# Performance work log

Measured on AMD Instinct MI355X. Metric: run time of the kernel, lower is better.

## Reference

```python
import jax, jax.numpy as jnp
import numpy as np

B, N, DH, DX, DQ, DE = 8, 256, 32, 3, 1, 8
H1, H2 = 32, 32
DIN = 2 * (DX + DH + DQ) + DE  # 80
TOL = 1e-5


def setup_inputs() -> dict:
    key = jax.random.key(0)
    ks = jax.random.split(key, 11)
    s1 = 1.0 / np.sqrt(DIN)
    s2 = 1.0 / np.sqrt(H1)
    s3 = 1.0 / np.sqrt(H2)
    return {
        "h": jax.random.normal(ks[0], (B, N, DH), jnp.float32),
        "e": jax.random.uniform(ks[1], (B, N, N, DE), jnp.float32),
        "x": jax.random.normal(ks[2], (B, N, DX), jnp.float32),
        "q": jax.random.normal(ks[3], (B, N, DQ), jnp.float32),
        "mask": jax.random.uniform(ks[4], (B, N, N, 1), jnp.float32),
        "W1": jax.random.normal(ks[5], (DIN, H1), jnp.float32) * s1,
        "b1": jnp.zeros((H1,), jnp.float32),
        "W2": jax.random.normal(ks[6], (H1, H2), jnp.float32) * s2,
        "b2": jnp.zeros((H2,), jnp.float32),
        "W3": jax.random.normal(ks[7], (H2, 1), jnp.float32) * s3,
        "b3": jnp.zeros((1,), jnp.float32),
    }


def reference(h, e, x, q, mask, W1, b1, W2, b2, W3, b3):
    natom = e.shape[1]
    # is_near: any edge feature above tolerance for pair (i,j)
    clip = jnp.clip(e, TOL, 1e5)
    is_near = (jnp.max(clip, axis=-1) != TOL).astype(jnp.float32)  # [B,N,N]
    m = jnp.max(mask, axis=-1)  # [B,N,N]

    def mlp(z):  # [..., DIN] -> [...]
        z = jax.nn.relu(z @ W1 + b1)
        z = jax.nn.relu(z @ W2 + b2)
        return (z @ W3 + b3)[..., 0]

    inp_atom = jnp.concatenate([x, h, q], axis=-1)  # [B,N,F]
    F = inp_atom.shape[-1]
    inp_i = jnp.broadcast_to(inp_atom[:, :, None, :], (inp_atom.shape[0], natom, natom, F))
    inp_j = jnp.transpose(inp_i, (0, 2, 1, 3))

    elec_ij = mlp(jnp.concatenate([inp_i, inp_j, e], axis=-1))  # [B,N,N]
    elec_ji = mlp(jnp.concatenate([inp_j, inp_i, e], axis=-1))  # [B,N,N]

    antisym = 0.5 * (elec_ij - elec_ji) * m * is_near
    q = q + jnp.sum(antisym, axis=2)[..., None]  # [B,N,1]
    return q
```

## Files before the change

kernel.cpp:

```cpp
#include <hip/hip_runtime.h>


#define NATOM 256
#define TOT_ATOMS 2048
#define ZS 40

typedef __bf16 bf16x8 __attribute__((ext_vector_type(8)));
typedef float  f32x16 __attribute__((ext_vector_type(16)));

__device__ __forceinline__ unsigned int pk2(float a, float b) {
    unsigned short lo = __builtin_bit_cast(unsigned short, (__bf16)a);
    unsigned short hi = __builtin_bit_cast(unsigned short, (__bf16)b);
    return (unsigned int)lo | ((unsigned int)hi << 16);
}

__global__ __launch_bounds__(256) void atom_proj_kernel(
    const float* __restrict__ x, const float* __restrict__ h,
    const float* __restrict__ q, const float* __restrict__ W1,
    const float* __restrict__ b1, float* __restrict__ P)
{
    const int a  = threadIdx.x >> 5;
    const int u  = threadIdx.x & 31;
    const int n0 = blockIdx.x * 8;

    __shared__ float sd[8][37];
    for (int idx = threadIdx.x; idx < 8 * 36; idx += 256) {
        const int aa = idx / 36, r = idx - aa * 36;
        const int n = n0 + aa;
        float v;
        if (r < 3)       v = x[n * 3 + r];
        else if (r < 35) v = h[n * 32 + (r - 3)];
        else             v = q[n];
        sd[aa][r] = v;
    }
    __syncthreads();

    float pa = 0.f, pb = b1[u];
#pragma unroll
    for (int r = 0; r < 36; ++r) {
        const float d = sd[a][r];
        pa += d * W1[r * 32 + u];
        pb += d * W1[(36 + r) * 32 + u];
    }
    const int n = n0 + a;
    P[(size_t)n * 64 + u]      = pa;
    P[(size_t)n * 64 + 32 + u] = pb;
}

__global__ __launch_bounds__(256, 3) void pair_kernel(
    const float* __restrict__ e, const float* __restrict__ mask,
    const float* __restrict__ q, const float* __restrict__ P,
    const float* __restrict__ W1, const float* __restrict__ W2,
    const float* __restrict__ b2, const float* __restrict__ W3,
    float* __restrict__ out)
{
    const int row = blockIdx.x;
    const int b   = row >> 8;
    const int j   = threadIdx.x;
    const int col = (b << 8) + j;

    __shared__ unsigned short Zij[256 * ZS];
    __shared__ unsigned short Zji[256 * ZS];
    __shared__ unsigned short W2t[32 * ZS];
    __shared__ float g_lds[256];
    __shared__ float red[4];

    const float* ep = e + (size_t)(row * NATOM + j) * 8;
    const float4 ev0 = ((const float4*)ep)[0];
    const float4 ev1 = ((const float4*)ep)[1];
    float e8[8] = {ev0.x, ev0.y, ev0.z, ev0.w, ev1.x, ev1.y, ev1.z, ev1.w};
    const float m = mask[row * NATOM + j];
    float mx = e8[0];
#pragma unroll
    for (int k = 1; k < 8; ++k) mx = fmaxf(mx, e8[k]);
    const float near = (mx > 1e-5f) ? 1.0f : 0.0f;
    g_lds[j] = 0.5f * m * near;

    {
        const int u  = threadIdx.x >> 3;
        const int k0 = (threadIdx.x & 7) * 4;
        const unsigned int p0 = pk2(W2[(k0 + 0) * 32 + u], W2[(k0 + 1) * 32 + u]);
        const unsigned int p1 = pk2(W2[(k0 + 2) * 32 + u], W2[(k0 + 3) * 32 + u]);
        *(unsigned int*)&W2t[u * ZS + k0]     = p0;
        *(unsigned int*)&W2t[u * ZS + k0 + 2] = p1;
    }

    const float* Pi = P + (size_t)row * 64;
    const float* Pj = P + (size_t)col * 64;
#pragma unroll
    for (int kq = 0; kq < 8; ++kq) {
        const float4 paj4 = ((const float4*)Pj)[kq];
        const float4 pbj4 = ((const float4*)Pj)[8 + kq];
        const float* paj = (const float*)&paj4;
        const float* pbj = (const float*)&pbj4;
        float zij[4], zji[4];
#pragma unroll
        for (int kk = 0; kk < 4; ++kk) {
            const int k = kq * 4 + kk;
            float ez = 0.f;
#pragma unroll
            for (int de = 0; de < 8; ++de)
                ez += e8[de] * W1[(72 + de) * 32 + k];
            const float pai = Pi[k];
            const float pbi = Pi[32 + k];
            zij[kk] = fmaxf(pai + pbj[kk] + ez, 0.f);
            zji[kk] = fmaxf(paj[kk] + pbi + ez, 0.f);
        }
        const unsigned int i0 = pk2(zij[0], zij[1]), i1 = pk2(zij[2], zij[3]);
        const unsigned int j0 = pk2(zji[0], zji[1]), j1 = pk2(zji[2], zji[3]);
        *(uint2*)&Zij[j * ZS + kq * 4] = make_uint2(i0, i1);
        *(uint2*)&Zji[j * ZS + kq * 4] = make_uint2(j0, j1);
    }
    __syncthreads();

    const int wave = threadIdx.x >> 6;
    const int lane = threadIdx.x & 63;
    const int lo = lane & 31;
    const int h  = lane >> 5;

    const bf16x8 a0 = *(const bf16x8*)&W2t[lo * ZS + h * 8];
    const bf16x8 a1 = *(const bf16x8*)&W2t[lo * ZS + 16 + h * 8];

    float vacc = 0.f;
#pragma unroll
    for (int nt = 0; nt < 2; ++nt) {
        const int jt = (wave + nt * 4) * 32;
        const int zo = (jt + lo) * ZS + h * 8;
        f32x16 cij = {0.f}, cji = {0.f};
        {
            const bf16x8 bz0 = *(const bf16x8*)&Zij[zo];
            const bf16x8 bz1 = *(const bf16x8*)&Zij[zo + 16];
            cij = __builtin_amdgcn_mfma_f32_32x32x16_bf16(a0, bz0, cij, 0, 0, 0);
            cij = __builtin_amdgcn_mfma_f32_32x32x16_bf16(a1, bz1, cij, 0, 0, 0);
        }
        {
            const bf16x8 bz0 = *(const bf16x8*)&Zji[zo];
            const bf16x8 bz1 = *(const bf16x8*)&Zji[zo + 16];
            cji = __builtin_amdgcn_mfma_f32_32x32x16_bf16(a0, bz0, cji, 0, 0, 0);
            cji = __builtin_amdgcn_mfma_f32_32x32x16_bf16(a1, bz1, cji, 0, 0, 0);
        }
        float d = 0.f;
#pragma unroll
        for (int reg = 0; reg < 16; ++reg) {
            const int u0 = (reg & 3) + 8 * (reg >> 2);
            const float b2v = h ? b2[u0 + 4] : b2[u0];
            const float w3v = h ? W3[u0 + 4] : W3[u0];
            const float rij = fmaxf(cij[reg] + b2v, 0.f);
            const float rji = fmaxf(cji[reg] + b2v, 0.f);
            d += (rij - rji) * w3v;
        }
        d += __shfl_xor(d, 32, 64);
        vacc += d * g_lds[jt + lo];
    }

#pragma unroll
    for (int off = 1; off < 64; off <<= 1)
        vacc += __shfl_xor(vacc, off, 64);
    if (lane == 0) red[wave] = vacc;
    __syncthreads();
    if (threadIdx.x == 0)
        out[row] = q[row] + 0.5f * (red[0] + red[1] + red[2] + red[3]);
}

extern "C" void kernel_launch(void* const* d_in, const int* in_sizes, int n_in,
                              void* d_out, int out_size, void* d_ws, size_t ws_size,
                              hipStream_t stream)
{
    const float* h    = (const float*)d_in[0];
    const float* e    = (const float*)d_in[1];
    const float* x    = (const float*)d_in[2];
    const float* q    = (const float*)d_in[3];
    const float* mask = (const float*)d_in[4];
    const float* W1   = (const float*)d_in[5];
    const float* b1   = (const float*)d_in[6];
    const float* W2   = (const float*)d_in[7];
    const float* b2   = (const float*)d_in[8];
    const float* W3   = (const float*)d_in[9];

    float* P = (float*)d_ws;

    atom_proj_kernel<<<256, 256, 0, stream>>>(x, h, q, W1, b1, P);
    pair_kernel<<<TOT_ATOMS, 256, 0, stream>>>(e, mask, q, P, W1, W2, b2, W3,
                                               (float*)d_out);
}
```

Measured before the change: 107.2 us.

## Build MFMA B-operands directly in registers, removing LDS staging of hidden activations

The first-layer activations are now computed directly in the lane layout that the 32x32x16 bf16 MFMA expects, so they feed the matrix op from registers instead of going through LDS with a block barrier. W2 fragments are loaded straight from global memory per lane. The launch-bounds occupancy hint rises from 3 to 4 blocks. The cost is duplicated e/mask loads and P loads across lane halves, plus higher register pressure.

```diff
diff --git a/kernel.cpp b/kernel.cpp
--- a/kernel.cpp
+++ b/kernel.cpp
@@ -3,16 +3,9 @@
 
 #define NATOM 256
 #define TOT_ATOMS 2048
-#define ZS 40
 
 typedef __bf16 bf16x8 __attribute__((ext_vector_type(8)));
 typedef float  f32x16 __attribute__((ext_vector_type(16)));
-
-__device__ __forceinline__ unsigned int pk2(float a, float b) {
-    unsigned short lo = __builtin_bit_cast(unsigned short, (__bf16)a);
-    unsigned short hi = __builtin_bit_cast(unsigned short, (__bf16)b);
-    return (unsigned int)lo | ((unsigned int)hi << 16);
-}
 
 __global__ __launch_bounds__(256) void atom_proj_kernel(
     const float* __restrict__ x, const float* __restrict__ h,
@@ -47,98 +40,94 @@
     P[(size_t)n * 64 + 32 + u] = pb;
 }
 
-__global__ __launch_bounds__(256, 3) void pair_kernel(
+__global__ __launch_bounds__(256, 4) void pair_kernel(
     const float* __restrict__ e, const float* __restrict__ mask,
     const float* __restrict__ q, const float* __restrict__ P,
     const float* __restrict__ W1, const float* __restrict__ W2,
     const float* __restrict__ b2, const float* __restrict__ W3,
     float* __restrict__ out)
 {
-    const int row = blockIdx.x;
-    const int b   = row >> 8;
-    const int j   = threadIdx.x;
-    const int col = (b << 8) + j;
+    const int row  = blockIdx.x;
+    const int b    = row >> 8;
+    const int tid  = threadIdx.x;
+    const int wave = tid >> 6;
+    const int lane = tid & 63;
+    const int lo   = lane & 31;
+    const int h    = lane >> 5;
 
-    __shared__ unsigned short Zij[256 * ZS];
-    __shared__ unsigned short Zji[256 * ZS];
-    __shared__ unsigned short W2t[32 * ZS];
-    __shared__ float g_lds[256];
-    __shared__ float red[4];
-
-    const float* ep = e + (size_t)(row * NATOM + j) * 8;
-    const float4 ev0 = ((const float4*)ep)[0];
-    const float4 ev1 = ((const float4*)ep)[1];
-    float e8[8] = {ev0.x, ev0.y, ev0.z, ev0.w, ev1.x, ev1.y, ev1.z, ev1.w};
-    const float m = mask[row * NATOM + j];
-    float mx = e8[0];
+    bf16x8 A0, A1;
 #pragma unroll
-    for (int k = 1; k < 8; ++k) mx = fmaxf(mx, e8[k]);
-    const float near = (mx > 1e-5f) ? 1.0f : 0.0f;
-    g_lds[j] = 0.5f * m * near;
-
-    {
-        const int u  = threadIdx.x >> 3;
-        const int k0 = (threadIdx.x & 7) * 4;
-        const unsigned int p0 = pk2(W2[(k0 + 0) * 32 + u], W2[(k0 + 1) * 32 + u]);
-        const unsigned int p1 = pk2(W2[(k0 + 2) * 32 + u], W2[(k0 + 3) * 32 + u]);
-        *(unsigned int*)&W2t[u * ZS + k0]     = p0;
-        *(unsigned int*)&W2t[u * ZS + k0 + 2] = p1;
+    for (int t = 0; t < 8; ++t) {
+        A0[t] = (__bf16)W2[(h * 8 + t) * 32 + lo];
+        A1[t] = (__bf16)W2[(16 + h * 8 + t) * 32 + lo];
     }
 
     const float* Pi = P + (size_t)row * 64;
-    const float* Pj = P + (size_t)col * 64;
+    __shared__ float red[4];
+    float vacc = 0.f;
+
 #pragma unroll
-    for (int kq = 0; kq < 8; ++kq) {
-        const float4 paj4 = ((const float4*)Pj)[kq];
-        const float4 pbj4 = ((const float4*)Pj)[8 + kq];
-        const float* paj = (const float*)&paj4;
-        const float* pbj = (const float*)&pbj4;
-        float zij[4], zji[4];
+    for (int st = 0; st < 2; ++st) {
+        const int j    = (wave << 6) + (st << 5) + lo;
+        const int colj = (b << 8) + j;
+        const float* Pj = P + (size_t)colj * 64;
+
+        const float* ep = e + ((size_t)row * NATOM + j) * 8;
+        float e8[8];
+        *(float4*)&e8[0] = ((const float4*)ep)[0];
+        *(float4*)&e8[4] = ((const float4*)ep)[1];
+        const float m = mask[row * NATOM + j];
+        float mx = e8[0];
 #pragma unroll
-        for (int kk = 0; kk < 4; ++kk) {
-            const int k = kq * 4 + kk;
-            float ez = 0.f;
+        for (int k = 1; k < 8; ++k) mx = fmaxf(mx, e8[k]);
+        const float g = (mx > 1e-5f) ? 0.5f * m : 0.f;
+
+        f32x16 cij = {0.f}, cji = {0.f};
 #pragma unroll
-            for (int de = 0; de < 8; ++de)
-                ez += e8[de] * W1[(72 + de) * 32 + k];
-            const float pai = Pi[k];
-            const float pbi = Pi[32 + k];
-            zij[kk] = fmaxf(pai + pbj[kk] + ez, 0.f);
-            zji[kk] = fmaxf(paj[kk] + pbi + ez, 0.f);
+        for (int kb = 0; kb < 2; ++kb) {
+            const int k0 = kb * 16 + h * 8;
+            const float4 pai0 = *(const float4*)(Pi + k0);
+            const float4 pai1 = *(const float4*)(Pi + k0 + 4);
+            const float4 pbi0 = *(const float4*)(Pi + 32 + k0);
+            const float4 pbi1 = *(const float4*)(Pi + 32 + k0 + 4);
+            const float4 paj0 = *(const float4*)(Pj + k0);
+            const float4 paj1 = *(const float4*)(Pj + k0 + 4);
+            const float4 pbj0 = *(const float4*)(Pj + 32 + k0);
+            const float4 pbj1 = *(const float4*)(Pj + 32 + k0 + 4);
+
+            float ez[8] = {0.f, 0.f, 0.f, 0.f, 0.f, 0.f, 0.f, 0.f};
+#pragma unroll
+            for (int de = 0; de < 8; ++de) {
+                const float ev = e8[de];
+                const float4 wa = *(const float4*)(W1 + (72 + de) * 32 + k0);
+                const float4 wb = *(const float4*)(W1 + (72 + de) * 32 + k0 + 4);
+                ez[0] += ev * wa.x; ez[1] += ev * wa.y;
+                ez[2] += ev * wa.z; ez[3] += ev * wa.w;
+                ez[4] += ev * wb.x; ez[5] += ev * wb.y;
+                ez[6] += ev * wb.z; ez[7] += ev * wb.w;
+            }
+
+            bf16x8 Bij, Bji;
+#pragma unroll
+            for (int t = 0; t < 8; ++t) {
+                const float pai = (t < 4) ? ((const float*)&pai0)[t] : ((const float*)&pai1)[t - 4];
+                const float pbi = (t < 4) ? ((const float*)&pbi0)[t] : ((const float*)&pbi1)[t - 4];
+                const float paj = (t < 4) ? ((const float*)&paj0)[t] : ((const float*)&paj1)[t - 4];
+                const float pbj = (t < 4) ? ((const float*)&pbj0)[t] : ((const float*)&pbj1)[t - 4];
+                const float zij = fmaxf(pai + pbj + ez[t], 0.f);
+                const float zji = fmaxf(paj + pbi + ez[t], 0.f);
+                Bij[t] = (__bf16)zij;
+                Bji[t] = (__bf16)zji;
+            }
+            if (kb == 0) {
+                cij = __builtin_amdgcn_mfma_f32_32x32x16_bf16(A0, Bij, cij, 0, 0, 0);
+                cji = __builtin_amdgcn_mfma_f32_32x32x16_bf16(A0, Bji, cji, 0, 0, 0);
+            } else {
+                cij = __builtin_amdgcn_mfma_f32_32x32x16_bf16(A1, Bij, cij, 0, 0, 0);
+                cji = __builtin_amdgcn_mfma_f32_32x32x16_bf16(A1, Bji, cji, 0, 0, 0);
+            }
         }
-        const unsigned int i0 = pk2(zij[0], zij[1]), i1 = pk2(zij[2], zij[3]);
-        const unsigned int j0 = pk2(zji[0], zji[1]), j1 = pk2(zji[2], zji[3]);
-        *(uint2*)&Zij[j * ZS + kq * 4] = make_uint2(i0, i1);
-        *(uint2*)&Zji[j * ZS + kq * 4] = make_uint2(j0, j1);
-    }
-    __syncthreads();
 
-    const int wave = threadIdx.x >> 6;
-    const int lane = threadIdx.x & 63;
-    const int lo = lane & 31;
-    const int h  = lane >> 5;
-
-    const bf16x8 a0 = *(const bf16x8*)&W2t[lo * ZS + h * 8];
-    const bf16x8 a1 = *(const bf16x8*)&W2t[lo * ZS + 16 + h * 8];
-
-    float vacc = 0.f;
-#pragma unroll
-    for (int nt = 0; nt < 2; ++nt) {
-        const int jt = (wave + nt * 4) * 32;
-        const int zo = (jt + lo) * ZS + h * 8;
-        f32x16 cij = {0.f}, cji = {0.f};
-        {
-            const bf16x8 bz0 = *(const bf16x8*)&Zij[zo];
-            const bf16x8 bz1 = *(const bf16x8*)&Zij[zo + 16];
-            cij = __builtin_amdgcn_mfma_f32_32x32x16_bf16(a0, bz0, cij, 0, 0, 0);
-            cij = __builtin_amdgcn_mfma_f32_32x32x16_bf16(a1, bz1, cij, 0, 0, 0);
-        }
-        {
-            const bf16x8 bz0 = *(const bf16x8*)&Zji[zo];
-            const bf16x8 bz1 = *(const bf16x8*)&Zji[zo + 16];
-            cji = __builtin_amdgcn_mfma_f32_32x32x16_bf16(a0, bz0, cji, 0, 0, 0);
-            cji = __builtin_amdgcn_mfma_f32_32x32x16_bf16(a1, bz1, cji, 0, 0, 0);
-        }
         float d = 0.f;
 #pragma unroll
         for (int reg = 0; reg < 16; ++reg) {
@@ -150,7 +139,7 @@
             d += (rij - rji) * w3v;
         }
         d += __shfl_xor(d, 32, 64);
-        vacc += d * g_lds[jt + lo];
+        vacc += d * g;
     }
 
 #pragma unroll
@@ -158,7 +147,7 @@
         vacc += __shfl_xor(vacc, off, 64);
     if (lane == 0) red[wave] = vacc;
     __syncthreads();
-    if (threadIdx.x == 0)
+    if (tid == 0)
         out[row] = q[row] + 0.5f * (red[0] + red[1] + red[2] + red[3]);
 }
 
```

After: 315.4 us. +194.2%, slower.

## Swizzle unpadded Z tiles in LDS and load W2 fragments directly to registers

Applied to the files above, without the earlier changes.

Removes the padding from the Z row stride and applies an XOR swizzle to the 8-element chunks so the bf16x8 reads avoid LDS bank conflicts while using less shared memory. The transposed W2 staging in LDS is dropped. Each lane now builds its MFMA A operand straight from global W2 into registers. Occupancy is raised to 4 blocks per SIMD in launch bounds, which adds register pressure.

```diff
diff --git a/kernel.cpp b/kernel.cpp
--- a/kernel.cpp
+++ b/kernel.cpp
@@ -3,10 +3,13 @@
 
 #define NATOM 256
 #define TOT_ATOMS 2048
-#define ZS 40
+#define ZS 32
 
 typedef __bf16 bf16x8 __attribute__((ext_vector_type(8)));
 typedef float  f32x16 __attribute__((ext_vector_type(16)));
+typedef float  f32x4  __attribute__((ext_vector_type(4)));
+typedef unsigned int u32x2 __attribute__((ext_vector_type(2)));
+typedef unsigned int u32x4 __attribute__((ext_vector_type(4)));
 
 __device__ __forceinline__ unsigned int pk2(float a, float b) {
     unsigned short lo = __builtin_bit_cast(unsigned short, (__bf16)a);
@@ -47,7 +50,7 @@
     P[(size_t)n * 64 + 32 + u] = pb;
 }
 
-__global__ __launch_bounds__(256, 3) void pair_kernel(
+__global__ __launch_bounds__(256, 4) void pair_kernel(
     const float* __restrict__ e, const float* __restrict__ mask,
     const float* __restrict__ q, const float* __restrict__ P,
     const float* __restrict__ W1, const float* __restrict__ W2,
@@ -61,83 +64,82 @@
 
     __shared__ unsigned short Zij[256 * ZS];
     __shared__ unsigned short Zji[256 * ZS];
-    __shared__ unsigned short W2t[32 * ZS];
     __shared__ float g_lds[256];
     __shared__ float red[4];
 
-    const float* ep = e + (size_t)(row * NATOM + j) * 8;
-    const float4 ev0 = ((const float4*)ep)[0];
-    const float4 ev1 = ((const float4*)ep)[1];
-    float e8[8] = {ev0.x, ev0.y, ev0.z, ev0.w, ev1.x, ev1.y, ev1.z, ev1.w};
+    const float* ep = e + ((size_t)row * NATOM + j) * 8;
+    const f32x4 ea = *(const f32x4*)(ep);
+    const f32x4 eb = *(const f32x4*)(ep + 4);
     const float m = mask[row * NATOM + j];
-    float mx = e8[0];
-#pragma unroll
-    for (int k = 1; k < 8; ++k) mx = fmaxf(mx, e8[k]);
-    const float near = (mx > 1e-5f) ? 1.0f : 0.0f;
-    g_lds[j] = 0.5f * m * near;
-
-    {
-        const int u  = threadIdx.x >> 3;
-        const int k0 = (threadIdx.x & 7) * 4;
-        const unsigned int p0 = pk2(W2[(k0 + 0) * 32 + u], W2[(k0 + 1) * 32 + u]);
-        const unsigned int p1 = pk2(W2[(k0 + 2) * 32 + u], W2[(k0 + 3) * 32 + u]);
-        *(unsigned int*)&W2t[u * ZS + k0]     = p0;
-        *(unsigned int*)&W2t[u * ZS + k0 + 2] = p1;
-    }
+    const float mx = fmaxf(fmaxf(fmaxf(ea[0], ea[1]), fmaxf(ea[2], ea[3])),
+                           fmaxf(fmaxf(eb[0], eb[1]), fmaxf(eb[2], eb[3])));
+    g_lds[j] = (mx > 1e-5f) ? 0.5f * m : 0.f;
 
     const float* Pi = P + (size_t)row * 64;
     const float* Pj = P + (size_t)col * 64;
+    const int sw = (j >> 1) & 3;
 #pragma unroll
     for (int kq = 0; kq < 8; ++kq) {
-        const float4 paj4 = ((const float4*)Pj)[kq];
-        const float4 pbj4 = ((const float4*)Pj)[8 + kq];
-        const float* paj = (const float*)&paj4;
-        const float* pbj = (const float*)&pbj4;
+        const f32x4 paj = *(const f32x4*)(Pj + kq * 4);
+        const f32x4 pbj = *(const f32x4*)(Pj + 32 + kq * 4);
         float zij[4], zji[4];
 #pragma unroll
         for (int kk = 0; kk < 4; ++kk) {
             const int k = kq * 4 + kk;
             float ez = 0.f;
 #pragma unroll
-            for (int de = 0; de < 8; ++de)
-                ez += e8[de] * W1[(72 + de) * 32 + k];
+            for (int de = 0; de < 8; ++de) {
+                const float ev = (de < 4) ? ea[de] : eb[de - 4];
+                ez += ev * W1[(72 + de) * 32 + k];
+            }
             const float pai = Pi[k];
             const float pbi = Pi[32 + k];
             zij[kk] = fmaxf(pai + pbj[kk] + ez, 0.f);
             zji[kk] = fmaxf(paj[kk] + pbi + ez, 0.f);
         }
-        const unsigned int i0 = pk2(zij[0], zij[1]), i1 = pk2(zij[2], zij[3]);
-        const unsigned int j0 = pk2(zji[0], zji[1]), j1 = pk2(zji[2], zji[3]);
-        *(uint2*)&Zij[j * ZS + kq * 4] = make_uint2(i0, i1);
-        *(uint2*)&Zji[j * ZS + kq * 4] = make_uint2(j0, j1);
+        const int off = j * ZS + (((kq >> 1) ^ sw) << 3) + ((kq & 1) << 2);
+        *(u32x2*)&Zij[off] = (u32x2){ pk2(zij[0], zij[1]), pk2(zij[2], zij[3]) };
+        *(u32x2*)&Zji[off] = (u32x2){ pk2(zji[0], zji[1]), pk2(zji[2], zji[3]) };
     }
-    __syncthreads();
 
     const int wave = threadIdx.x >> 6;
     const int lane = threadIdx.x & 63;
-    const int lo = lane & 31;
-    const int h  = lane >> 5;
+    const int lo   = lane & 31;
+    const int h    = lane >> 5;
+    const int kA   = h * 8;
+    const u32x4 a0w = { pk2(W2[(kA + 0) * 32 + lo], W2[(kA + 1) * 32 + lo]),
+                        pk2(W2[(kA + 2) * 32 + lo], W2[(kA + 3) * 32 + lo]),
+                        pk2(W2[(kA + 4) * 32 + lo], W2[(kA + 5) * 32 + lo]),
+                        pk2(W2[(kA + 6) * 32 + lo], W2[(kA + 7) * 32 + lo]) };
+    const u32x4 a1w = { pk2(W2[(16 + kA + 0) * 32 + lo], W2[(16 + kA + 1) * 32 + lo]),
+                        pk2(W2[(16 + kA + 2) * 32 + lo], W2[(16 + kA + 3) * 32 + lo]),
+                        pk2(W2[(16 + kA + 4) * 32 + lo], W2[(16 + kA + 5) * 32 + lo]),
+                        pk2(W2[(16 + kA + 6) * 32 + lo], W2[(16 + kA + 7) * 32 + lo]) };
+    const bf16x8 A0 = __builtin_bit_cast(bf16x8, a0w);
+    const bf16x8 A1 = __builtin_bit_cast(bf16x8, a1w);
 
-    const bf16x8 a0 = *(const bf16x8*)&W2t[lo * ZS + h * 8];
-    const bf16x8 a1 = *(const bf16x8*)&W2t[lo * ZS + 16 + h * 8];
+    __syncthreads();
 
+    const int swr = (lo >> 1) & 3;
     float vacc = 0.f;
 #pragma unroll
     for (int nt = 0; nt < 2; ++nt) {
         const int jt = (wave + nt * 4) * 32;
-        const int zo = (jt + lo) * ZS + h * 8;
+        const int rbase = (jt + lo) * ZS;
+        const int o0 = rbase + (((0 * 2 + h) ^ swr) << 3);
+        const int o1 = rbase + (((1 * 2 + h) ^ swr) << 3);
         f32x16 cij = {0.f}, cji = {0.f};
         {
-            const bf16x8 bz0 = *(const bf16x8*)&Zij[zo];
-            const bf16x8 bz1 = *(const bf16x8*)&Zij[zo + 16];
-            cij = __builtin_amdgcn_mfma_f32_32x32x16_bf16(a0, bz0, cij, 0, 0, 0);
-            cij = __builtin_amdgcn_mfma_f32_32x32x16_bf16(a1, bz1, cij, 0, 0, 0);
+            const bf16x8 bz0 = *(const bf16x8*)&Zij[o0];
+            const bf16x8 bz1 = *(const bf16x8*)&Zij[o1];
+            cij = __builtin_amdgcn_mfma_f32_32x32x16_bf16(A0, bz0, cij, 0, 0, 0);
+            cij = __builtin_amdgcn_mfma_f32_32x32x16_bf16(A1, bz1, cij, 0, 0, 0);
         }
         {
-            const bf16x8 bz0 = *(const bf16x8*)&Zji[zo];
-            const bf16x8 bz1 = *(const bf16x8*)&Zji[zo + 16];
-            cji = __builtin_amdgcn_mfma_f32_32x32x16_bf16(a0, bz0, cji, 0, 0, 0);
-            cji = __builtin_amdgcn_mfma_f32_32x32x16_bf16(a1, bz1, cji, 0, 0, 0);
+            const bf16x8 bz0 = *(const bf16x8*)&Zji[o0];
+            const bf16x8 bz1 = *(const bf16x8*)&Zji[o1];
+            cji = __builtin_amdgcn_mfma_f32_32x32x16_bf16(A0, bz0, cji, 0, 0, 0);
+            cji = __builtin_amdgcn_mfma_f32_32x32x16_bf16(A1, bz1, cji, 0, 0, 0);
         }
         float d = 0.f;
 #pragma unroll
```

Result: slower. 135.4 us (+26.3%).
